# Kernel optimization log

Hardware: AMD Instinct MI355X
Metric: run time of the kernel (lower is better)

Reference implementation:

```python
import jax, jax.numpy as jnp
import numpy as np

B, N, C = 2048, 128, 128
H = 4
NW = 64


def setup_inputs() -> dict:
    key = jax.random.key(0)
    ks = jax.random.split(key, 6)
    return {
        "x": jax.random.normal(ks[0], (B, N, C), dtype=jnp.float32),
        "mask": jax.random.normal(ks[1], (NW, N, N), dtype=jnp.float32),
        "qkv_w": jax.random.normal(ks[2], (3 * C, C), dtype=jnp.float32) * (C ** -0.5),
        "qkv_b": jax.random.normal(ks[3], (3 * C,), dtype=jnp.float32) * 0.02,
        "proj_w": jax.random.normal(ks[4], (C, C), dtype=jnp.float32) * (C ** -0.5),
        "proj_b": jax.random.normal(ks[5], (C,), dtype=jnp.float32) * 0.02,
    }


def reference(x, mask, qkv_w, qkv_b, proj_w, proj_b):
    b, n, c = x.shape
    h = H
    hd = c // h
    scale = hd ** -0.5
    # qkv projection: [B,N,3C] -> [3,B,H,N,hd]
    qkv = (x @ qkv_w.T + qkv_b).reshape(b, n, 3, h, hd).transpose(2, 0, 3, 1, 4)
    q, k, v = qkv[0], qkv[1], qkv[2]
    # scores [B,H,N,N]
    attn = jnp.einsum("bhnd,bhmd->bhnm", q, k) * scale
    nw = mask.shape[0]
    # add per-window mask: view as [B//nW, nW, H, N, N] + mask[None,:,None]
    attn = attn.reshape(b // nw, nw, h, n, n) + mask[None, :, None, :, :]
    attn = attn.reshape(b, h, n, n)
    attn = jax.nn.softmax(attn, axis=-1)
    out = jnp.einsum("bhnm,bhmd->bhnd", attn, v)
    out = out.transpose(0, 2, 1, 3).reshape(b, n, c)
    out = out @ proj_w.T + proj_b
    return out
```

## Files before the change

kernel.cpp:

```cpp
#include <hip/hip_runtime.h>

typedef __bf16 bf16x8 __attribute__((ext_vector_type(8)));
typedef __bf16 bf16x4 __attribute__((ext_vector_type(4)));
typedef float  f32x4  __attribute__((ext_vector_type(4)));

__device__ __forceinline__ int swz(int row, int colb) {
    return row * 256 + (colb ^ ((row & 7) << 4));
}
__device__ __forceinline__ int pswz(int row, int colb) {
    return row * 128 + (colb ^ ((row & 7) << 4));
}

__global__ void prep_weights(const float* __restrict__ qkv_w,
                             const float* __restrict__ proj_w,
                             __bf16* __restrict__ wq, __bf16* __restrict__ wp) {
    int i = blockIdx.x * 256 + threadIdx.x;
    wq[i] = (__bf16)qkv_w[i];
    if (i < 16384) wp[i] = (__bf16)proj_w[i];
}

#define A_LDS_X   0
#define A_LDS_P   0
#define A_LDS_Q   32768
#define A_LDS_K   49152
#define A_LDS_VT  65536
#define A_LDS_TOTAL 81920

__global__ void __launch_bounds__(512, 4)
attn_split(const float* __restrict__ x, const float* __restrict__ mask,
           const float* __restrict__ qkv_b,
           const __bf16* __restrict__ wq,
           __bf16* __restrict__ Og) {
    extern __shared__ char smem[];
    const int b    = blockIdx.x >> 1;
    const int hp   = blockIdx.x & 1;
    const int tid  = threadIdx.x;
    const int wave = tid >> 6;
    const int lane = tid & 63;
    const int l16  = lane & 15;
    const int lg   = lane >> 4;

    {
        const float* xb = x + (size_t)b * 16384;
        #pragma unroll
        for (int it = 0; it < 4; ++it) {
            int i   = it * 512 + tid;
            int row = i >> 4;
            int c8  = (i & 15) << 3;
            float4 f0 = *(const float4*)(xb + row * 128 + c8);
            float4 f1 = *(const float4*)(xb + row * 128 + c8 + 4);
            bf16x8 v;
            v[0] = (__bf16)f0.x; v[1] = (__bf16)f0.y; v[2] = (__bf16)f0.z; v[3] = (__bf16)f0.w;
            v[4] = (__bf16)f1.x; v[5] = (__bf16)f1.y; v[6] = (__bf16)f1.z; v[7] = (__bf16)f1.w;
            *(bf16x8*)(smem + A_LDS_X + swz(row, c8 * 2)) = v;
        }
    }
    __syncthreads();

    {
        const int g  = wave >> 1;
        const int nh = wave & 1;
        const int f0 = g * 48;
        f32x4 acc[3][4];
        #pragma unroll
        for (int jt = 0; jt < 3; ++jt)
            #pragma unroll
            for (int nt = 0; nt < 4; ++nt)
                acc[jt][nt] = {0.f, 0.f, 0.f, 0.f};
        int jg_t[3];
        #pragma unroll
        for (int jt = 0; jt < 3; ++jt) {
            int ft = f0 + jt * 16;
            jg_t[jt] = (ft < 64) ? (hp * 64 + ft)
                     : (ft < 128) ? (128 + hp * 64 + (ft - 64))
                                  : (256 + hp * 64 + (ft - 128));
        }
        #pragma unroll
        for (int kc = 0; kc < 4; ++kc) {
            bf16x8 afr[3];
            #pragma unroll
            for (int jt = 0; jt < 3; ++jt)
                afr[jt] = *(const bf16x8*)(wq + (jg_t[jt] + l16) * 128 + kc * 32 + lg * 8);
            bf16x8 bfr[4];
            #pragma unroll
            for (int nt = 0; nt < 4; ++nt)
                bfr[nt] = *(const bf16x8*)(smem + A_LDS_X +
                            swz((nh * 4 + nt) * 16 + l16, (kc * 32 + lg * 8) * 2));
            #pragma unroll
            for (int jt = 0; jt < 3; ++jt)
                #pragma unroll
                for (int nt = 0; nt < 4; ++nt)
                    acc[jt][nt] = __builtin_amdgcn_mfma_f32_16x16x32_bf16(
                                      afr[jt], bfr[nt], acc[jt][nt], 0, 0, 0);
        }
        #pragma unroll
        for (int jt = 0; jt < 3; ++jt) {
            int f = f0 + jt * 16 + lg * 4;
            float4 bias = *(const float4*)(qkv_b + jg_t[jt] + lg * 4);
            #pragma unroll
            for (int nt = 0; nt < 4; ++nt) {
                int n = (nh * 4 + nt) * 16 + l16;
                f32x4 a = acc[jt][nt];
                __bf16 e0 = (__bf16)(a[0] + bias.x);
                __bf16 e1 = (__bf16)(a[1] + bias.y);
                __bf16 e2 = (__bf16)(a[2] + bias.z);
                __bf16 e3 = (__bf16)(a[3] + bias.w);
                if (f < 64) {
                    bf16x4 v4 = {e0, e1, e2, e3};
                    *(bf16x4*)(smem + A_LDS_Q + pswz(n, f * 2)) = v4;
                } else if (f < 128) {
                    bf16x4 v4 = {e0, e1, e2, e3};
                    *(bf16x4*)(smem + A_LDS_K + pswz(n, (f - 64) * 2)) = v4;
                } else {
                    int d = f - 128;
                    *(__bf16*)(smem + A_LDS_VT + swz(d + 0, n * 2)) = e0;
                    *(__bf16*)(smem + A_LDS_VT + swz(d + 1, n * 2)) = e1;
                    *(__bf16*)(smem + A_LDS_VT + swz(d + 2, n * 2)) = e2;
                    *(__bf16*)(smem + A_LDS_VT + swz(d + 3, n * 2)) = e3;
                }
            }
        }
    }
    __syncthreads();

    const int hl = wave >> 2;
    const int q4 = wave & 3;
    const int hgl = hp * 2 + hl;
    const float sc = 0.17677669529663687f;
    bf16x8 kfr[8];
    #pragma unroll
    for (int mt = 0; mt < 8; ++mt)
        kfr[mt] = *(const bf16x8*)(smem + A_LDS_K +
                      pswz(mt * 16 + l16, (hl * 32 + lg * 8) * 2));
    bf16x8 vfr[2][4];
    #pragma unroll
    for (int dt = 0; dt < 2; ++dt)
        #pragma unroll
        for (int kc = 0; kc < 4; ++kc)
            vfr[dt][kc] = *(const bf16x8*)(smem + A_LDS_VT +
                            swz(hl * 32 + dt * 16 + l16, (kc * 32 + lg * 8) * 2));

    const float* mwin = mask + (size_t)(b & 63) * 16384;
    char* pbase = smem + A_LDS_P + wave * 4096;

    #pragma unroll
    for (int i = 0; i < 2; ++i) {
        const int nt = q4 * 2 + i;
        bf16x8 qfr = *(const bf16x8*)(smem + A_LDS_Q +
                        pswz(nt * 16 + l16, (hl * 32 + lg * 8) * 2));
        f32x4 s[8];
        #pragma unroll
        for (int mt = 0; mt < 8; ++mt) {
            f32x4 z = {0.f, 0.f, 0.f, 0.f};
            s[mt] = __builtin_amdgcn_mfma_f32_16x16x32_bf16(kfr[mt], qfr, z, 0, 0, 0);
        }
        const float* mrow = mwin + (size_t)(nt * 16 + l16) * 128;
        #pragma unroll
        for (int mt = 0; mt < 8; ++mt) {
            float4 mk = *(const float4*)(mrow + mt * 16 + lg * 4);
            s[mt][0] = fmaf(s[mt][0], sc, mk.x);
            s[mt][1] = fmaf(s[mt][1], sc, mk.y);
            s[mt][2] = fmaf(s[mt][2], sc, mk.z);
            s[mt][3] = fmaf(s[mt][3], sc, mk.w);
        }
        f32x4 vm0 = s[0], vm1 = s[1];
        #pragma unroll
        for (int mt = 2; mt < 8; mt += 2) {
            vm0[0]=fmaxf(vm0[0],s[mt][0]); vm0[1]=fmaxf(vm0[1],s[mt][1]);
            vm0[2]=fmaxf(vm0[2],s[mt][2]); vm0[3]=fmaxf(vm0[3],s[mt][3]);
            vm1[0]=fmaxf(vm1[0],s[mt+1][0]); vm1[1]=fmaxf(vm1[1],s[mt+1][1]);
            vm1[2]=fmaxf(vm1[2],s[mt+1][2]); vm1[3]=fmaxf(vm1[3],s[mt+1][3]);
        }
        float mx = fmaxf(fmaxf(fmaxf(vm0[0],vm1[0]), fmaxf(vm0[1],vm1[1])),
                         fmaxf(fmaxf(vm0[2],vm1[2]), fmaxf(vm0[3],vm1[3])));
        mx = fmaxf(mx, __shfl_xor(mx, 16));
        mx = fmaxf(mx, __shfl_xor(mx, 32));
        f32x4 vs = {0.f, 0.f, 0.f, 0.f};
        #pragma unroll
        for (int mt = 0; mt < 8; ++mt) {
            #pragma unroll
            for (int r = 0; r < 4; ++r) {
                float p = __expf(s[mt][r] - mx);
                s[mt][r] = p;
                vs[r] += p;
            }
        }
        float sm = (vs[0] + vs[1]) + (vs[2] + vs[3]);
        sm += __shfl_xor(sm, 16);
        sm += __shfl_xor(sm, 32);
        float inv = 1.f / sm;
        #pragma unroll
        for (int mt = 0; mt < 8; ++mt) {
            bf16x4 pv = {(__bf16)s[mt][0], (__bf16)s[mt][1],
                         (__bf16)s[mt][2], (__bf16)s[mt][3]};
            *(bf16x4*)(pbase + swz(l16, mt * 32 + lg * 8)) = pv;
        }
        bf16x8 pafr[4];
        #pragma unroll
        for (int kc = 0; kc < 4; ++kc)
            pafr[kc] = *(const bf16x8*)(pbase + swz(l16, kc * 64 + lg * 16));
        f32x4 o[2];
        o[0] = {0.f, 0.f, 0.f, 0.f};
        o[1] = {0.f, 0.f, 0.f, 0.f};
        #pragma unroll
        for (int kc = 0; kc < 4; ++kc) {
            o[0] = __builtin_amdgcn_mfma_f32_16x16x32_bf16(vfr[0][kc], pafr[kc], o[0], 0, 0, 0);
            o[1] = __builtin_amdgcn_mfma_f32_16x16x32_bf16(vfr[1][kc], pafr[kc], o[1], 0, 0, 0);
        }
        __bf16* og = Og + ((size_t)b * 128 + nt * 16 + l16) * 128 + hgl * 32 + lg * 4;
        #pragma unroll
        for (int dt = 0; dt < 2; ++dt) {
            bf16x4 ov = {(__bf16)(o[dt][0] * inv), (__bf16)(o[dt][1] * inv),
                         (__bf16)(o[dt][2] * inv), (__bf16)(o[dt][3] * inv)};
            *(bf16x4*)(og + dt * 16) = ov;
        }
    }
}

__global__ void __launch_bounds__(256)
proj_out(const __bf16* __restrict__ Og, const __bf16* __restrict__ wp,
         const float* __restrict__ proj_b, float* __restrict__ out) {
    const int b    = blockIdx.x;
    const int tid  = threadIdx.x;
    const int wave = tid >> 6;
    const int l16  = tid & 15;
    const int lg   = (tid & 63) >> 4;

    f32x4 facc[2][8];
    #pragma unroll
    for (int nt2 = 0; nt2 < 2; ++nt2)
        #pragma unroll
        for (int ct = 0; ct < 8; ++ct)
            facc[nt2][ct] = {0.f, 0.f, 0.f, 0.f};
    #pragma unroll
    for (int kc = 0; kc < 4; ++kc) {
        bf16x8 ofr[2];
        #pragma unroll
        for (int nt2 = 0; nt2 < 2; ++nt2)
            ofr[nt2] = *(const bf16x8*)(Og +
                          ((size_t)b * 128 + wave * 32 + nt2 * 16 + l16) * 128 +
                          kc * 32 + lg * 8);
        bf16x8 wfr[8];
        #pragma unroll
        for (int ct = 0; ct < 8; ++ct)
            wfr[ct] = *(const bf16x8*)(wp + (ct * 16 + l16) * 128 + kc * 32 + lg * 8);
        #pragma unroll
        for (int nt2 = 0; nt2 < 2; ++nt2)
            #pragma unroll
            for (int ct = 0; ct < 8; ++ct)
                facc[nt2][ct] = __builtin_amdgcn_mfma_f32_16x16x32_bf16(
                                    wfr[ct], ofr[nt2], facc[nt2][ct], 0, 0, 0);
    }
    float* ob = out + (size_t)b * 16384;
    #pragma unroll
    for (int ct = 0; ct < 8; ++ct) {
        float4 pb4 = *(const float4*)(proj_b + ct * 16 + lg * 4);
        #pragma unroll
        for (int nt2 = 0; nt2 < 2; ++nt2) {
            int n = wave * 32 + nt2 * 16 + l16;
            float4 ov;
            ov.x = facc[nt2][ct][0] + pb4.x;
            ov.y = facc[nt2][ct][1] + pb4.y;
            ov.z = facc[nt2][ct][2] + pb4.z;
            ov.w = facc[nt2][ct][3] + pb4.w;
            *(float4*)(ob + n * 128 + ct * 16 + lg * 4) = ov;
        }
    }
}

#define LDS_XO 0
#define LDS_Q  32768
#define LDS_K  65536
#define LDS_VT 98304
#define LDS_P  131072
#define LDS_TOTAL 147456

__global__ void __launch_bounds__(512, 2)
attn_fused(const float* __restrict__ x, const float* __restrict__ mask,
           const float* __restrict__ qkv_b, const float* __restrict__ proj_b,
           const __bf16* __restrict__ wq, const __bf16* __restrict__ wp,
           float* __restrict__ out) {
    extern __shared__ char smem[];
    const int b    = blockIdx.x;
    const int tid  = threadIdx.x;
    const int wave = tid >> 6;
    const int lane = tid & 63;
    const int l16  = lane & 15;
    const int lg   = lane >> 4;

    {
        const float* xb = x + (size_t)b * 16384;
        #pragma unroll
        for (int it = 0; it < 4; ++it) {
            int i   = it * 512 + tid;
            int row = i >> 4;
            int c8  = (i & 15) << 3;
            float4 f0 = *(const float4*)(xb + row * 128 + c8);
            float4 f1 = *(const float4*)(xb + row * 128 + c8 + 4);
            bf16x8 v;
            v[0] = (__bf16)f0.x; v[1] = (__bf16)f0.y; v[2] = (__bf16)f0.z; v[3] = (__bf16)f0.w;
            v[4] = (__bf16)f1.x; v[5] = (__bf16)f1.y; v[6] = (__bf16)f1.z; v[7] = (__bf16)f1.w;
            *(bf16x8*)(smem + LDS_XO + swz(row, c8 * 2)) = v;
        }
    }
    __syncthreads();

    const int j0 = wave * 48;
    #pragma unroll
    for (int pass = 0; pass < 2; ++pass) {
        f32x4 acc[3][4];
        #pragma unroll
        for (int jt = 0; jt < 3; ++jt)
            #pragma unroll
            for (int nt = 0; nt < 4; ++nt)
                acc[jt][nt] = {0.f, 0.f, 0.f, 0.f};
        #pragma unroll
        for (int kc = 0; kc < 4; ++kc) {
            bf16x8 afr[3];
            #pragma unroll
            for (int jt = 0; jt < 3; ++jt)
                afr[jt] = *(const bf16x8*)(wq + (j0 + jt * 16 + l16) * 128 + kc * 32 + lg * 8);
            bf16x8 bfr[4];
            #pragma unroll
            for (int nt = 0; nt < 4; ++nt)
                bfr[nt] = *(const bf16x8*)(smem + LDS_XO +
                            swz((pass * 4 + nt) * 16 + l16, (kc * 32 + lg * 8) * 2));
            #pragma unroll
            for (int jt = 0; jt < 3; ++jt)
                #pragma unroll
                for (int nt = 0; nt < 4; ++nt)
                    acc[jt][nt] = __builtin_amdgcn_mfma_f32_16x16x32_bf16(
                                      afr[jt], bfr[nt], acc[jt][nt], 0, 0, 0);
        }
        #pragma unroll
        for (int jt = 0; jt < 3; ++jt) {
            int jbase = j0 + jt * 16 + lg * 4;
            float4 bias = *(const float4*)(qkv_b + jbase);
            #pragma unroll
            for (int nt = 0; nt < 4; ++nt) {
                int n = (pass * 4 + nt) * 16 + l16;
                f32x4 a = acc[jt][nt];
                __bf16 e0 = (__bf16)(a[0] + bias.x);
                __bf16 e1 = (__bf16)(a[1] + bias.y);
                __bf16 e2 = (__bf16)(a[2] + bias.z);
                __bf16 e3 = (__bf16)(a[3] + bias.w);
                if (jbase < 128) {
                    bf16x4 v4 = {e0, e1, e2, e3};
                    *(bf16x4*)(smem + LDS_Q + swz(n, jbase * 2)) = v4;
                } else if (jbase < 256) {
                    bf16x4 v4 = {e0, e1, e2, e3};
                    *(bf16x4*)(smem + LDS_K + swz(n, (jbase - 128) * 2)) = v4;
                } else {
                    int d = jbase - 256;
                    *(__bf16*)(smem + LDS_VT + swz(d + 0, n * 2)) = e0;
                    *(__bf16*)(smem + LDS_VT + swz(d + 1, n * 2)) = e1;
                    *(__bf16*)(smem + LDS_VT + swz(d + 2, n * 2)) = e2;
                    *(__bf16*)(smem + LDS_VT + swz(d + 3, n * 2)) = e3;
                }
            }
        }
    }
    __syncthreads();

    const int h  = wave >> 1;
    const int rh = wave & 1;
    const float sc = 0.17677669529663687f;
    bf16x8 kfr[8];
    #pragma unroll
    for (int mt = 0; mt < 8; ++mt)
        kfr[mt] = *(const bf16x8*)(smem + LDS_K + swz(mt * 16 + l16, (h * 32 + lg * 8) * 2));
    bf16x8 vfr[2][4];
    #pragma unroll
    for (int dt = 0; dt < 2; ++dt)
        #pragma unroll
        for (int kc = 0; kc < 4; ++kc)
            vfr[dt][kc] = *(const bf16x8*)(smem + LDS_VT +
                            swz(h * 32 + dt * 16 + l16, (kc * 32 + lg * 8) * 2));

    const float* mwin = mask + (size_t)(b & 63) * 16384;
    char* pbase = smem + LDS_P + wave * 2048;

    #pragma unroll
    for (int i = 0; i < 4; ++i) {
        const int nt = rh * 4 + i;
        bf16x8 qfr = *(const bf16x8*)(smem + LDS_Q + swz(nt * 16 + l16, (h * 32 + lg * 8) * 2));
        f32x4 s[8];
        #pragma unroll
        for (int mt = 0; mt < 8; ++mt) {
            f32x4 z = {0.f, 0.f, 0.f, 0.f};
            s[mt] = __builtin_amdgcn_mfma_f32_16x16x32_bf16(qfr, kfr[mt], z, 0, 0, 0);
        }
        float mx[4] = {-1e30f, -1e30f, -1e30f, -1e30f};
        #pragma unroll
        for (int mt = 0; mt < 8; ++mt)
            #pragma unroll
            for (int r = 0; r < 4; ++r) {
                float v = s[mt][r] * sc + mwin[(nt * 16 + lg * 4 + r) * 128 + mt * 16 + l16];
                s[mt][r] = v;
                mx[r] = fmaxf(mx[r], v);
            }
        #pragma unroll
        for (int r = 0; r < 4; ++r) {
            float m = mx[r];
            m = fmaxf(m, __shfl_xor(m, 1));
            m = fmaxf(m, __shfl_xor(m, 2));
            m = fmaxf(m, __shfl_xor(m, 4));
            m = fmaxf(m, __shfl_xor(m, 8));
            mx[r] = m;
        }
        float sm[4] = {0.f, 0.f, 0.f, 0.f};
        #pragma unroll
        for (int mt = 0; mt < 8; ++mt)
            #pragma unroll
            for (int r = 0; r < 4; ++r) {
                float p = __expf(s[mt][r] - mx[r]);
                s[mt][r] = p;
                sm[r] += p;
            }
        #pragma unroll
        for (int r = 0; r < 4; ++r) {
            float t = sm[r];
            t += __shfl_xor(t, 1);
            t += __shfl_xor(t, 2);
            t += __shfl_xor(t, 4);
            t += __shfl_xor(t, 8);
            sm[r] = 1.f / t;
        }
        f32x4 o[2];
        o[0] = {0.f, 0.f, 0.f, 0.f};
        o[1] = {0.f, 0.f, 0.f, 0.f};
        #pragma unroll
        for (int hp2 = 0; hp2 < 2; ++hp2) {
            #pragma unroll
            for (int mtl = 0; mtl < 4; ++mtl) {
                int mt = hp2 * 4 + mtl;
                #pragma unroll
                for (int r = 0; r < 4; ++r)
                    *(__bf16*)(pbase + pswz(lg * 4 + r, (mtl * 16 + l16) * 2)) =
                        (__bf16)(s[mt][r] * sm[r]);
            }
            #pragma unroll
            for (int q = 0; q < 2; ++q) {
                int kc = hp2 * 2 + q;
                bf16x8 pafr = *(const bf16x8*)(pbase + pswz(l16, (q * 32 + lg * 8) * 2));
                #pragma unroll
                for (int dt = 0; dt < 2; ++dt)
                    o[dt] = __builtin_amdgcn_mfma_f32_16x16x32_bf16(
                                pafr, vfr[dt][kc], o[dt], 0, 0, 0);
            }
        }
        #pragma unroll
        for (int dt = 0; dt < 2; ++dt)
            #pragma unroll
            for (int r = 0; r < 4; ++r)
                *(__bf16*)(smem + LDS_XO +
                    swz(nt * 16 + lg * 4 + r, (h * 32 + dt * 16 + l16) * 2)) = (__bf16)o[dt][r];
    }
    __syncthreads();

    f32x4 facc[8];
    #pragma unroll
    for (int ct = 0; ct < 8; ++ct)
        facc[ct] = {0.f, 0.f, 0.f, 0.f};
    #pragma unroll
    for (int kc = 0; kc < 4; ++kc) {
        bf16x8 afr = *(const bf16x8*)(smem + LDS_XO +
                        swz(wave * 16 + l16, (kc * 32 + lg * 8) * 2));
        bf16x8 bfr[8];
        #pragma unroll
        for (int ct = 0; ct < 8; ++ct)
            bfr[ct] = *(const bf16x8*)(wp + (ct * 16 + l16) * 128 + kc * 32 + lg * 8);
        #pragma unroll
        for (int ct = 0; ct < 8; ++ct)
            facc[ct] = __builtin_amdgcn_mfma_f32_16x16x32_bf16(
                           afr, bfr[ct], facc[ct], 0, 0, 0);
    }
    float* ob = out + (size_t)b * 16384;
    #pragma unroll
    for (int ct = 0; ct < 8; ++ct) {
        float pb = proj_b[ct * 16 + l16];
        int n0 = wave * 16 + lg * 4;
        #pragma unroll
        for (int r = 0; r < 4; ++r)
            ob[(n0 + r) * 128 + ct * 16 + l16] = facc[ct][r] + pb;
    }
}

extern "C" void kernel_launch(void* const* d_in, const int* in_sizes, int n_in,
                              void* d_out, int out_size, void* d_ws, size_t ws_size,
                              hipStream_t stream) {
    const float* x      = (const float*)d_in[0];
    const float* mask   = (const float*)d_in[1];
    const float* qkv_w  = (const float*)d_in[2];
    const float* qkv_b  = (const float*)d_in[3];
    const float* proj_w = (const float*)d_in[4];
    const float* proj_b = (const float*)d_in[5];
    float* out = (float*)d_out;

    __bf16* wq = (__bf16*)d_ws;
    __bf16* wp = wq + 49152;

    prep_weights<<<192, 256, 0, stream>>>(qkv_w, proj_w, wq, wp);

    const size_t og_bytes = (size_t)2048 * 128 * 128 * 2;
    const size_t need = 131072 + og_bytes;

    if (ws_size >= need) {
        __bf16* Og = (__bf16*)((char*)d_ws + 131072);
        hipFuncSetAttribute((const void*)attn_split,
                            hipFuncAttributeMaxDynamicSharedMemorySize, A_LDS_TOTAL);
        attn_split<<<4096, 512, A_LDS_TOTAL, stream>>>(x, mask, qkv_b, wq, Og);
        proj_out<<<2048, 256, 0, stream>>>(Og, wp, proj_b, out);
    } else {
        hipFuncSetAttribute((const void*)attn_fused,
                            hipFuncAttributeMaxDynamicSharedMemorySize, LDS_TOTAL);
        attn_fused<<<2048, 512, LDS_TOTAL, stream>>>(x, mask, qkv_b, proj_b, wq, wp, out);
    }
}
```

Measured before the change: 417.3 us.

## Split attention kernel per head with direct global x loads into MFMA fragments

Replaces the two-heads-per-block attention kernel with a one-head-per-block kernel of 256 threads and 40KB LDS, launched as 8192 blocks. x is now read from global memory and converted to bf16 straight into MFMA fragments instead of being staged through LDS, and mask loads are issued before the QK MFMAs to hide latency. Smaller blocks and less LDS should allow more resident blocks and less synchronisation. In exchange, each x tile is reread and reconverted by four blocks instead of two, which adds global traffic.

```diff
diff --git a/kernel.cpp b/kernel.cpp
--- a/kernel.cpp
+++ b/kernel.cpp
@@ -19,149 +19,130 @@
     if (i < 16384) wp[i] = (__bf16)proj_w[i];
 }
 
-#define A_LDS_X   0
-#define A_LDS_P   0
-#define A_LDS_Q   32768
-#define A_LDS_K   49152
-#define A_LDS_VT  65536
-#define A_LDS_TOTAL 81920
-
-__global__ void __launch_bounds__(512, 4)
-attn_split(const float* __restrict__ x, const float* __restrict__ mask,
-           const float* __restrict__ qkv_b,
-           const __bf16* __restrict__ wq,
-           __bf16* __restrict__ Og) {
+#define H_LDS_QK  0
+#define H_LDS_VT  16384
+#define H_LDS_P   24576
+#define H_LDS_TOTAL 40960
+
+__global__ void __launch_bounds__(256, 4)
+attn_head(const float* __restrict__ x, const float* __restrict__ mask,
+          const float* __restrict__ qkv_b,
+          const __bf16* __restrict__ wq,
+          __bf16* __restrict__ Og) {
     extern __shared__ char smem[];
-    const int b    = blockIdx.x >> 1;
-    const int hp   = blockIdx.x & 1;
+    const int b    = blockIdx.x >> 2;
+    const int h    = blockIdx.x & 3;
     const int tid  = threadIdx.x;
     const int wave = tid >> 6;
     const int lane = tid & 63;
     const int l16  = lane & 15;
     const int lg   = lane >> 4;
 
+    const float* xb = x + (size_t)b * 16384;
+
     {
-        const float* xb = x + (size_t)b * 16384;
-        #pragma unroll
-        for (int it = 0; it < 4; ++it) {
-            int i   = it * 512 + tid;
-            int row = i >> 4;
-            int c8  = (i & 15) << 3;
-            float4 f0 = *(const float4*)(xb + row * 128 + c8);
-            float4 f1 = *(const float4*)(xb + row * 128 + c8 + 4);
-            bf16x8 v;
-            v[0] = (__bf16)f0.x; v[1] = (__bf16)f0.y; v[2] = (__bf16)f0.z; v[3] = (__bf16)f0.w;
-            v[4] = (__bf16)f1.x; v[5] = (__bf16)f1.y; v[6] = (__bf16)f1.z; v[7] = (__bf16)f1.w;
-            *(bf16x8*)(smem + A_LDS_X + swz(row, c8 * 2)) = v;
-        }
-    }
-    __syncthreads();
-
-    {
-        const int g  = wave >> 1;
-        const int nh = wave & 1;
-        const int f0 = g * 48;
-        f32x4 acc[3][4];
-        #pragma unroll
-        for (int jt = 0; jt < 3; ++jt)
-            #pragma unroll
-            for (int nt = 0; nt < 4; ++nt)
-                acc[jt][nt] = {0.f, 0.f, 0.f, 0.f};
-        int jg_t[3];
-        #pragma unroll
-        for (int jt = 0; jt < 3; ++jt) {
-            int ft = f0 + jt * 16;
-            jg_t[jt] = (ft < 64) ? (hp * 64 + ft)
-                     : (ft < 128) ? (128 + hp * 64 + (ft - 64))
-                                  : (256 + hp * 64 + (ft - 128));
-        }
+        f32x4 acc[6][2];
+        #pragma unroll
+        for (int jt = 0; jt < 6; ++jt)
+            #pragma unroll
+            for (int t = 0; t < 2; ++t)
+                acc[jt][t] = {0.f, 0.f, 0.f, 0.f};
+        int jg_t[6];
+        #pragma unroll
+        for (int jt = 0; jt < 6; ++jt)
+            jg_t[jt] = (jt < 2) ? (h * 32 + jt * 16)
+                     : (jt < 4) ? (128 + h * 32 + (jt - 2) * 16)
+                                : (256 + h * 32 + (jt - 4) * 16);
         #pragma unroll
         for (int kc = 0; kc < 4; ++kc) {
-            bf16x8 afr[3];
-            #pragma unroll
-            for (int jt = 0; jt < 3; ++jt)
+            bf16x8 bfr[2];
+            #pragma unroll
+            for (int t = 0; t < 2; ++t) {
+                const float* src = xb + ((wave * 2 + t) * 16 + l16) * 128 + kc * 32 + lg * 8;
+                float4 u0 = *(const float4*)(src);
+                float4 u1 = *(const float4*)(src + 4);
+                bf16x8 v;
+                v[0] = (__bf16)u0.x; v[1] = (__bf16)u0.y; v[2] = (__bf16)u0.z; v[3] = (__bf16)u0.w;
+                v[4] = (__bf16)u1.x; v[5] = (__bf16)u1.y; v[6] = (__bf16)u1.z; v[7] = (__bf16)u1.w;
+                bfr[t] = v;
+            }
+            bf16x8 afr[6];
+            #pragma unroll
+            for (int jt = 0; jt < 6; ++jt)
                 afr[jt] = *(const bf16x8*)(wq + (jg_t[jt] + l16) * 128 + kc * 32 + lg * 8);
-            bf16x8 bfr[4];
-            #pragma unroll
-            for (int nt = 0; nt < 4; ++nt)
-                bfr[nt] = *(const bf16x8*)(smem + A_LDS_X +
-                            swz((nh * 4 + nt) * 16 + l16, (kc * 32 + lg * 8) * 2));
-            #pragma unroll
-            for (int jt = 0; jt < 3; ++jt)
+            #pragma unroll
+            for (int jt = 0; jt < 6; ++jt)
                 #pragma unroll
-                for (int nt = 0; nt < 4; ++nt)
-                    acc[jt][nt] = __builtin_amdgcn_mfma_f32_16x16x32_bf16(
-                                      afr[jt], bfr[nt], acc[jt][nt], 0, 0, 0);
-        }
-        #pragma unroll
-        for (int jt = 0; jt < 3; ++jt) {
-            int f = f0 + jt * 16 + lg * 4;
+                for (int t = 0; t < 2; ++t)
+                    acc[jt][t] = __builtin_amdgcn_mfma_f32_16x16x32_bf16(
+                                     afr[jt], bfr[t], acc[jt][t], 0, 0, 0);
+        }
+        #pragma unroll
+        for (int jt = 0; jt < 6; ++jt) {
+            int f = jt * 16 + lg * 4;
             float4 bias = *(const float4*)(qkv_b + jg_t[jt] + lg * 4);
             #pragma unroll
-            for (int nt = 0; nt < 4; ++nt) {
-                int n = (nh * 4 + nt) * 16 + l16;
-                f32x4 a = acc[jt][nt];
+            for (int t = 0; t < 2; ++t) {
+                int n = (wave * 2 + t) * 16 + l16;
+                f32x4 a = acc[jt][t];
                 __bf16 e0 = (__bf16)(a[0] + bias.x);
                 __bf16 e1 = (__bf16)(a[1] + bias.y);
                 __bf16 e2 = (__bf16)(a[2] + bias.z);
                 __bf16 e3 = (__bf16)(a[3] + bias.w);
-                if (f < 64) {
+                if (jt < 4) {
                     bf16x4 v4 = {e0, e1, e2, e3};
-                    *(bf16x4*)(smem + A_LDS_Q + pswz(n, f * 2)) = v4;
-                } else if (f < 128) {
-                    bf16x4 v4 = {e0, e1, e2, e3};
-                    *(bf16x4*)(smem + A_LDS_K + pswz(n, (f - 64) * 2)) = v4;
+                    *(bf16x4*)(smem + H_LDS_QK + pswz(n, f * 2)) = v4;
                 } else {
-                    int d = f - 128;
-                    *(__bf16*)(smem + A_LDS_VT + swz(d + 0, n * 2)) = e0;
-                    *(__bf16*)(smem + A_LDS_VT + swz(d + 1, n * 2)) = e1;
-                    *(__bf16*)(smem + A_LDS_VT + swz(d + 2, n * 2)) = e2;
-                    *(__bf16*)(smem + A_LDS_VT + swz(d + 3, n * 2)) = e3;
+                    int d = f - 64;
+                    *(__bf16*)(smem + H_LDS_VT + swz(d + 0, n * 2)) = e0;
+                    *(__bf16*)(smem + H_LDS_VT + swz(d + 1, n * 2)) = e1;
+                    *(__bf16*)(smem + H_LDS_VT + swz(d + 2, n * 2)) = e2;
+                    *(__bf16*)(smem + H_LDS_VT + swz(d + 3, n * 2)) = e3;
                 }
             }
         }
     }
     __syncthreads();
 
-    const int hl = wave >> 2;
-    const int q4 = wave & 3;
-    const int hgl = hp * 2 + hl;
     const float sc = 0.17677669529663687f;
     bf16x8 kfr[8];
     #pragma unroll
     for (int mt = 0; mt < 8; ++mt)
-        kfr[mt] = *(const bf16x8*)(smem + A_LDS_K +
-                      pswz(mt * 16 + l16, (hl * 32 + lg * 8) * 2));
+        kfr[mt] = *(const bf16x8*)(smem + H_LDS_QK +
+                      pswz(mt * 16 + l16, (32 + lg * 8) * 2));
     bf16x8 vfr[2][4];
     #pragma unroll
     for (int dt = 0; dt < 2; ++dt)
         #pragma unroll
         for (int kc = 0; kc < 4; ++kc)
-            vfr[dt][kc] = *(const bf16x8*)(smem + A_LDS_VT +
-                            swz(hl * 32 + dt * 16 + l16, (kc * 32 + lg * 8) * 2));
+            vfr[dt][kc] = *(const bf16x8*)(smem + H_LDS_VT +
+                            swz(dt * 16 + l16, (kc * 32 + lg * 8) * 2));
 
     const float* mwin = mask + (size_t)(b & 63) * 16384;
-    char* pbase = smem + A_LDS_P + wave * 4096;
+    char* pbase = smem + H_LDS_P + wave * 4096;
 
     #pragma unroll
     for (int i = 0; i < 2; ++i) {
-        const int nt = q4 * 2 + i;
-        bf16x8 qfr = *(const bf16x8*)(smem + A_LDS_Q +
-                        pswz(nt * 16 + l16, (hl * 32 + lg * 8) * 2));
+        const int nt = wave * 2 + i;
+        const float* mrow = mwin + (size_t)(nt * 16 + l16) * 128;
+        float4 mk[8];
+        #pragma unroll
+        for (int mt = 0; mt < 8; ++mt)
+            mk[mt] = *(const float4*)(mrow + mt * 16 + lg * 4);
+        bf16x8 qfr = *(const bf16x8*)(smem + H_LDS_QK +
+                        pswz(nt * 16 + l16, (lg * 8) * 2));
         f32x4 s[8];
         #pragma unroll
         for (int mt = 0; mt < 8; ++mt) {
             f32x4 z = {0.f, 0.f, 0.f, 0.f};
             s[mt] = __builtin_amdgcn_mfma_f32_16x16x32_bf16(kfr[mt], qfr, z, 0, 0, 0);
         }
-        const float* mrow = mwin + (size_t)(nt * 16 + l16) * 128;
         #pragma unroll
         for (int mt = 0; mt < 8; ++mt) {
-            float4 mk = *(const float4*)(mrow + mt * 16 + lg * 4);
-            s[mt][0] = fmaf(s[mt][0], sc, mk.x);
-            s[mt][1] = fmaf(s[mt][1], sc, mk.y);
-            s[mt][2] = fmaf(s[mt][2], sc, mk.z);
-            s[mt][3] = fmaf(s[mt][3], sc, mk.w);
+            s[mt][0] = fmaf(s[mt][0], sc, mk[mt].x);
+            s[mt][1] = fmaf(s[mt][1], sc, mk[mt].y);
+            s[mt][2] = fmaf(s[mt][2], sc, mk[mt].z);
+            s[mt][3] = fmaf(s[mt][3], sc, mk[mt].w);
         }
         f32x4 vm0 = s[0], vm1 = s[1];
         #pragma unroll
@@ -207,7 +188,7 @@
             o[0] = __builtin_amdgcn_mfma_f32_16x16x32_bf16(vfr[0][kc], pafr[kc], o[0], 0, 0, 0);
             o[1] = __builtin_amdgcn_mfma_f32_16x16x32_bf16(vfr[1][kc], pafr[kc], o[1], 0, 0, 0);
         }
-        __bf16* og = Og + ((size_t)b * 128 + nt * 16 + l16) * 128 + hgl * 32 + lg * 4;
+        __bf16* og = Og + ((size_t)b * 128 + nt * 16 + l16) * 128 + h * 32 + lg * 4;
         #pragma unroll
         for (int dt = 0; dt < 2; ++dt) {
             bf16x4 ov = {(__bf16)(o[dt][0] * inv), (__bf16)(o[dt][1] * inv),
@@ -507,9 +488,9 @@
 
     if (ws_size >= need) {
         __bf16* Og = (__bf16*)((char*)d_ws + 131072);
-        hipFuncSetAttribute((const void*)attn_split,
-                            hipFuncAttributeMaxDynamicSharedMemorySize, A_LDS_TOTAL);
-        attn_split<<<4096, 512, A_LDS_TOTAL, stream>>>(x, mask, qkv_b, wq, Og);
+        hipFuncSetAttribute((const void*)attn_head,
+                            hipFuncAttributeMaxDynamicSharedMemorySize, H_LDS_TOTAL);
+        attn_head<<<8192, 256, H_LDS_TOTAL, stream>>>(x, mask, qkv_b, wq, Og);
         proj_out<<<2048, 256, 0, stream>>>(Og, wp, proj_b, out);
     } else {
         hipFuncSetAttribute((const void*)attn_fused,
```

Result: slower. 506.8 us (+21.5%).
